# Kernel tuning notes

Hardware: AMD Instinct MI355X
Metric: run time of the kernel (lower is better)

## Reference

```python
import jax, jax.numpy as jnp
import numpy as np

NUM_HEADS = 16


def setup_inputs() -> dict:
    key = jax.random.key(0)
    ks = jax.random.split(key, 5)
    B, N, D = 2, 2048, 1024
    scale = 1.0 / np.sqrt(D)  # roughly xavier-ish magnitude for weights
    return {
        "x": jax.random.normal(ks[0], (B, N, D), dtype=jnp.float32),
        "W_query": jax.random.normal(ks[1], (D, D), dtype=jnp.float32) * scale,
        "W_key": jax.random.normal(ks[2], (D, D), dtype=jnp.float32) * scale,
        "W_value": jax.random.normal(ks[3], (D, D), dtype=jnp.float32) * scale,
        "W_output": jax.random.normal(ks[4], (D, D), dtype=jnp.float32) * scale,
    }


def reference(x, W_query, W_key, W_value, W_output):
    # x: [B, N, D]; weights: [D, D]
    B, N, D = x.shape
    H = NUM_HEADS
    hd = D // H

    def mh_embed(W):
        # linear_embedding then split heads: [B, N, D] -> [B, H, N, hd]
        y = jnp.einsum("bnd,de->bne", x, W)
        return y.reshape(B, N, H, hd).transpose(0, 2, 1, 3)

    q = mh_embed(W_query)
    k = mh_embed(W_key)
    v = mh_embed(W_value)

    # NOTE: source scales by token_dim**-0.5 (full model dim), not head_dim
    attn = jnp.einsum("bhnd,bhmd->bhnm", q, k) * (D ** -0.5)
    attn = jax.nn.softmax(attn, axis=-1)
    out = jnp.einsum("bhnm,bhmd->bhnd", attn, v)  # [B, H, N, hd]

    out = out.transpose(0, 2, 1, 3).reshape(B, N, D)  # merge heads
    out = jnp.einsum("bnd,de->bne", out, W_output)
    return out
```

## Files before the change

### kernel.cpp

```cpp
#include <hip/hip_runtime.h>

#define D_MODEL 1024
#define N_TOK   2048
#define NHEAD   16
#define HDIM    64
#define BATCH   2
#define M_TOT   (BATCH*N_TOK)

typedef unsigned short u16;
typedef __bf16 bf16x8 __attribute__((ext_vector_type(8)));
typedef float  f32x4  __attribute__((ext_vector_type(4)));

#define QSCALE 0.04508422002777439f

__device__ __forceinline__ u16 f2bf(float f) {
  union { float f; unsigned u; } v; v.f = f;
  unsigned r = v.u + 0x7fffu + ((v.u >> 16) & 1u);
  return (u16)(r >> 16);
}

__device__ __forceinline__ float bf2f(u16 u) {
  union { unsigned u; float f; } v; v.u = ((unsigned)u) << 16; return v.f;
}

__device__ __forceinline__ unsigned pk2bf(float a, float b) {
#if __has_builtin(__builtin_amdgcn_cvt_pk_bf16_f32)
  typedef __bf16 bf16x2_t __attribute__((ext_vector_type(2)));
  bf16x2_t r = __builtin_amdgcn_cvt_pk_bf16_f32(a, b);
  union { bf16x2_t v; unsigned u; } c; c.v = r; return c.u;
#else
  return (unsigned)f2bf(a) | ((unsigned)f2bf(b) << 16);
#endif
}

__device__ __forceinline__ void gl2lds16(const void* g, void* l) {
  __builtin_amdgcn_global_load_lds(
      (__attribute__((address_space(1))) void*)g,
      (__attribute__((address_space(3))) void*)l, 16, 0, 0);
}

__global__ void prep_kernel(const float* __restrict__ x,
                            const float* __restrict__ s0, const float* __restrict__ s1,
                            const float* __restrict__ s2, const float* __restrict__ s3,
                            u16* __restrict__ xb,
                            u16* __restrict__ d0, u16* __restrict__ d1,
                            u16* __restrict__ d2, u16* __restrict__ d3) {
  const int t = threadIdx.y * 32 + threadIdx.x;
  if (blockIdx.z == 4) {
    int base = (blockIdx.y * 32 + blockIdx.x) * 256 + t;
#pragma unroll
    for (int r = 0; r < 4; ++r) {
      int i = base + r * 262144;
      float4 v = ((const float4*)x)[i];
      ushort4 o;
      o.x = f2bf(v.x); o.y = f2bf(v.y); o.z = f2bf(v.z); o.w = f2bf(v.w);
      ((ushort4*)xb)[i] = o;
    }
    return;
  }
  const float* src; u16* dst;
  switch (blockIdx.z) {
    case 0:  src = s0; dst = d0; break;
    case 1:  src = s1; dst = d1; break;
    case 2:  src = s2; dst = d2; break;
    default: src = s3; dst = d3; break;
  }
  float sc = (blockIdx.z == 0) ? QSCALE : 1.0f;
  __shared__ float tile[32][33];
  int xg = blockIdx.x * 32 + threadIdx.x;
  int ybase = blockIdx.y * 32;
#pragma unroll
  for (int r = 0; r < 4; ++r)
    tile[threadIdx.y + r*8][threadIdx.x] = src[(size_t)(ybase + threadIdx.y + r*8)*D_MODEL + xg];
  __syncthreads();
#pragma unroll
  for (int r = 0; r < 4; ++r)
    dst[(size_t)(blockIdx.x*32 + threadIdx.y + r*8)*D_MODEL + ybase + threadIdx.x] =
        f2bf(tile[threadIdx.x][threadIdx.y + r*8] * sc);
}

__device__ __forceinline__ void gemm_body(const u16* __restrict__ A,
                                          const u16* __restrict__ Bt,
                                          void* __restrict__ Cout, int mode) {
  __shared__ __attribute__((aligned(16))) u16 lA[2][128*32];
  __shared__ __attribute__((aligned(16))) u16 lB[2][128*32];
  const int t = threadIdx.x;
  const int lane = t & 63, w = t >> 6;
  const int wm = w >> 1, wn = w & 1;
  const int q4 = lane >> 4, l15 = lane & 15;
  const int m0 = blockIdx.y * 128, n0 = blockIdx.x * 128;

  const int c0 = t, c1 = 256 + t;
  const int r0 = c0 >> 2, g0 = (c0 & 3) ^ (r0 & 3);
  const int r1 = c1 >> 2, g1 = (c1 & 3) ^ (r1 & 3);

  f32x4 acc[4][4] = {};

  gl2lds16(A  + (size_t)(m0 + r0)*D_MODEL + g0*8, &lA[0][c0*8]);
  gl2lds16(Bt + (size_t)(n0 + r0)*D_MODEL + g0*8, &lB[0][c0*8]);
  gl2lds16(A  + (size_t)(m0 + r1)*D_MODEL + g1*8, &lA[0][c1*8]);
  gl2lds16(Bt + (size_t)(n0 + r1)*D_MODEL + g1*8, &lB[0][c1*8]);

  for (int it = 0; it < 32; ++it) {
    const int cur = it & 1;
    __syncthreads();
    if (it + 1 < 32) {
      const int kn = (it + 1) * 32;
      u16* dA = &lA[cur ^ 1][0]; u16* dB = &lB[cur ^ 1][0];
      gl2lds16(A  + (size_t)(m0 + r0)*D_MODEL + kn + g0*8, dA + c0*8);
      gl2lds16(Bt + (size_t)(n0 + r0)*D_MODEL + kn + g0*8, dB + c0*8);
      gl2lds16(A  + (size_t)(m0 + r1)*D_MODEL + kn + g1*8, dA + c1*8);
      gl2lds16(Bt + (size_t)(n0 + r1)*D_MODEL + kn + g1*8, dB + c1*8);
    }
    const u16* sA = &lA[cur][0]; const u16* sB = &lB[cur][0];
    bf16x8 af[4], bfr[4];
#pragma unroll
    for (int mi = 0; mi < 4; ++mi) {
      int r = wm*64 + mi*16 + l15;
      af[mi] = *(const bf16x8*)(sA + r*32 + ((q4 ^ (r & 3)) * 8));
    }
#pragma unroll
    for (int ni = 0; ni < 4; ++ni) {
      int r = wn*64 + ni*16 + l15;
      bfr[ni] = *(const bf16x8*)(sB + r*32 + ((q4 ^ (r & 3)) * 8));
    }
#pragma unroll
    for (int mi = 0; mi < 4; ++mi)
#pragma unroll
      for (int ni = 0; ni < 4; ++ni)
        acc[mi][ni] = __builtin_amdgcn_mfma_f32_16x16x32_bf16(af[mi], bfr[ni], acc[mi][ni], 0, 0, 0);
  }

#pragma unroll
  for (int mi = 0; mi < 4; ++mi) {
#pragma unroll
    for (int ni = 0; ni < 4; ++ni) {
      const int tok0 = m0 + wm*64 + mi*16 + q4*4;
      const int col  = n0 + wn*64 + ni*16 + l15;
      if (mode == 0) {
        u16* D = (u16*)Cout;
#pragma unroll
        for (int r = 0; r < 4; ++r) {
          int tok = tok0 + r;
          int b = tok >> 11, n = tok & (N_TOK-1);
          int h = col >> 6, d = col & (HDIM-1);
          D[(((size_t)(b*NHEAD + h))*N_TOK + n)*HDIM + d] = f2bf(acc[mi][ni][r]);
        }
      } else {
        int b = tok0 >> 11, n = tok0 & (N_TOK-1);
        int h = col >> 6, d = col & (HDIM-1);
        ushort4 pk;
        pk.x = f2bf(acc[mi][ni][0]); pk.y = f2bf(acc[mi][ni][1]);
        pk.z = f2bf(acc[mi][ni][2]); pk.w = f2bf(acc[mi][ni][3]);
        *(ushort4*)((u16*)Cout + ((size_t)(b*NHEAD + h)*HDIM + d)*N_TOK + n) = pk;
      }
    }
  }
}

__global__ __launch_bounds__(256) void qkv_kernel(const u16* __restrict__ xb,
    const u16* __restrict__ wqt, const u16* __restrict__ wkt, const u16* __restrict__ wvt,
    u16* __restrict__ Q, u16* __restrict__ K, u16* __restrict__ Vt) {
  int z = blockIdx.z;
  const u16* B = (z == 0) ? wqt : (z == 1) ? wkt : wvt;
  void* C = (z == 0) ? (void*)Q : (z == 1) ? (void*)K : (void*)Vt;
  gemm_body(xb, B, C, (z == 2) ? 2 : 0);
}

__global__ __launch_bounds__(256) void out_kernel(const u16* __restrict__ ctx,
    const u16* __restrict__ wot, float* __restrict__ out) {
  __shared__ __attribute__((aligned(16))) u16 lA[2][64*32];
  __shared__ __attribute__((aligned(16))) u16 lB[2][128*32];
  const int t = threadIdx.x;
  const int lane = t & 63, w = t >> 6;
  const int wm = w >> 1, wn = w & 1;
  const int q4 = lane >> 4, l15 = lane & 15;
  const int m0 = blockIdx.y * 64, n0 = blockIdx.x * 128;

  const int rA = t >> 2, gA = (t & 3) ^ (rA & 3);
  const int c0 = t, c1 = 256 + t;
  const int r0 = c0 >> 2, g0 = (c0 & 3) ^ (r0 & 3);
  const int r1 = c1 >> 2, g1 = (c1 & 3) ^ (r1 & 3);

  f32x4 acc[2][4] = {};

  gl2lds16(ctx + (size_t)(m0 + rA)*D_MODEL + gA*8, &lA[0][t*8]);
  gl2lds16(wot + (size_t)(n0 + r0)*D_MODEL + g0*8, &lB[0][c0*8]);
  gl2lds16(wot + (size_t)(n0 + r1)*D_MODEL + g1*8, &lB[0][c1*8]);

  for (int it = 0; it < 32; ++it) {
    const int cur = it & 1;
    __syncthreads();
    if (it + 1 < 32) {
      const int kn = (it + 1) * 32;
      u16* dA = &lA[cur ^ 1][0]; u16* dB = &lB[cur ^ 1][0];
      gl2lds16(ctx + (size_t)(m0 + rA)*D_MODEL + kn + gA*8, dA + t*8);
      gl2lds16(wot + (size_t)(n0 + r0)*D_MODEL + kn + g0*8, dB + c0*8);
      gl2lds16(wot + (size_t)(n0 + r1)*D_MODEL + kn + g1*8, dB + c1*8);
    }
    const u16* sA = &lA[cur][0]; const u16* sB = &lB[cur][0];
    bf16x8 af[2], bfr[4];
#pragma unroll
    for (int mi = 0; mi < 2; ++mi) {
      int r = wm*32 + mi*16 + l15;
      af[mi] = *(const bf16x8*)(sA + r*32 + ((q4 ^ (r & 3)) * 8));
    }
#pragma unroll
    for (int ni = 0; ni < 4; ++ni) {
      int r = wn*64 + ni*16 + l15;
      bfr[ni] = *(const bf16x8*)(sB + r*32 + ((q4 ^ (r & 3)) * 8));
    }
#pragma unroll
    for (int mi = 0; mi < 2; ++mi)
#pragma unroll
      for (int ni = 0; ni < 4; ++ni)
        acc[mi][ni] = __builtin_amdgcn_mfma_f32_16x16x32_bf16(af[mi], bfr[ni], acc[mi][ni], 0, 0, 0);
  }

#pragma unroll
  for (int mi = 0; mi < 2; ++mi) {
#pragma unroll
    for (int ni = 0; ni < 4; ++ni) {
      const int tok0 = m0 + wm*32 + mi*16 + q4*4;
      const int col  = n0 + wn*64 + ni*16 + l15;
#pragma unroll
      for (int r = 0; r < 4; ++r)
        out[(size_t)(tok0 + r)*D_MODEL + col] = acc[mi][ni][r];
    }
  }
}

__global__ __launch_bounds__(256, 4) void attn_kernel(const u16* __restrict__ Qg,
    const u16* __restrict__ Kg, const u16* __restrict__ Vtg,
    u16* __restrict__ Opart, float* __restrict__ Lpart) {
  __shared__ __attribute__((aligned(16))) u16 lds[16384];
  const int t = threadIdx.x;
  const int lane = t & 63, w = t >> 6;
  const int q4 = lane >> 4, l15 = lane & 15;
  const int q4sw = ((q4 & 1) << 1) | (q4 >> 1);
  const int bh = blockIdx.y;
  const int qb = blockIdx.x >> 1, half = blockIdx.x & 1;
  const int qw0 = qb * 128 + w * 32;
  const size_t kvBase = (size_t)bh * (N_TOK * HDIM);

  const int ck0 = t, ck1 = 256 + t;
  const int kr0 = ck0 >> 3, kg0 = (ck0 & 7) ^ (kr0 & 7);
  const int kr1 = ck1 >> 3, kg1 = (ck1 & 7) ^ (kr1 & 7);

  bf16x8 qf[2][2];
#pragma unroll
  for (int ni = 0; ni < 2; ++ni)
#pragma unroll
    for (int kk = 0; kk < 2; ++kk)
      qf[ni][kk] = *(const bf16x8*)(Qg + kvBase +
                    (size_t)(qw0 + ni*16 + l15)*HDIM + kk*32 + q4*8);

  f32x4 accO[4][2] = {};
  f32x4 accL[2] = {};
  const f32x4 fzero = {0.f, 0.f, 0.f, 0.f};
  union { unsigned uu[4]; bf16x8 v; } onesU;
  onesU.uu[0] = 0x3F803F80u; onesU.uu[1] = 0x3F803F80u;
  onesU.uu[2] = 0x3F803F80u; onesU.uu[3] = 0x3F803F80u;
  const bf16x8 ones = onesU.v;

  const int kvStart = half * 1024;
  gl2lds16(Kg  + kvBase + (size_t)(kvStart + kr0)*HDIM + kg0*8, lds + ck0*8);
  gl2lds16(Kg  + kvBase + (size_t)(kvStart + kr1)*HDIM + kg1*8, lds + ck1*8);
  gl2lds16(Vtg + kvBase + (size_t)kr0*N_TOK + kvStart + kg0*8,  lds + 8192 + ck0*8);
  gl2lds16(Vtg + kvBase + (size_t)kr1*N_TOK + kvStart + kg1*8,  lds + 8192 + ck1*8);

  for (int it = 0; it < 16; ++it) {
    const int cur = it & 1;
    __syncthreads();
    if (it + 1 < 16) {
      const int kvn = kvStart + (it + 1) * 64;
      u16* dK = lds + (cur ^ 1) * 4096;
      u16* dV = lds + 8192 + (cur ^ 1) * 4096;
      gl2lds16(Kg  + kvBase + (size_t)(kvn + kr0)*HDIM + kg0*8, dK + ck0*8);
      gl2lds16(Kg  + kvBase + (size_t)(kvn + kr1)*HDIM + kg1*8, dK + ck1*8);
      gl2lds16(Vtg + kvBase + (size_t)kr0*N_TOK + kvn + kg0*8,  dV + ck0*8);
      gl2lds16(Vtg + kvBase + (size_t)kr1*N_TOK + kvn + kg1*8,  dV + ck1*8);
    }
    const u16* sK = lds + cur * 4096;
    const u16* sV = lds + 8192 + cur * 4096;

    unsigned wv[4][2][2];
#pragma unroll
    for (int mip = 0; mip < 4; ++mip) {
      const int kv = mip*16 + l15;
      __builtin_amdgcn_s_setprio(1);
      bf16x8 a0 = *(const bf16x8*)(sK + kv*64 + (((q4    ) ^ (l15 & 7)) * 8));
      bf16x8 a1 = *(const bf16x8*)(sK + kv*64 + (((4 + q4) ^ (l15 & 7)) * 8));
      f32x4 s0, s1;
      s0 = __builtin_amdgcn_mfma_f32_16x16x32_bf16(a0, qf[0][0], fzero, 0, 0, 0);
      s1 = __builtin_amdgcn_mfma_f32_16x16x32_bf16(a0, qf[1][0], fzero, 0, 0, 0);
      s0 = __builtin_amdgcn_mfma_f32_16x16x32_bf16(a1, qf[0][1], s0, 0, 0, 0);
      s1 = __builtin_amdgcn_mfma_f32_16x16x32_bf16(a1, qf[1][1], s1, 0, 0, 0);
      __builtin_amdgcn_s_setprio(0);
      wv[mip][0][0] = pk2bf(__builtin_amdgcn_exp2f(s0[0]), __builtin_amdgcn_exp2f(s0[1]));
      wv[mip][0][1] = pk2bf(__builtin_amdgcn_exp2f(s0[2]), __builtin_amdgcn_exp2f(s0[3]));
      wv[mip][1][0] = pk2bf(__builtin_amdgcn_exp2f(s1[0]), __builtin_amdgcn_exp2f(s1[1]));
      wv[mip][1][1] = pk2bf(__builtin_amdgcn_exp2f(s1[2]), __builtin_amdgcn_exp2f(s1[3]));
    }

    bf16x8 bp[2][2];
#pragma unroll
    for (int ni = 0; ni < 2; ++ni)
#pragma unroll
      for (int kk2 = 0; kk2 < 2; ++kk2) {
        unsigned x0 = wv[2*kk2][ni][0], x1 = wv[2*kk2][ni][1];
        unsigned y0 = wv[2*kk2+1][ni][0], y1 = wv[2*kk2+1][ni][1];
        asm("v_permlane16_swap_b32 %0, %1" : "+v"(x0), "+v"(y0));
        asm("v_permlane16_swap_b32 %0, %1" : "+v"(x1), "+v"(y1));
        union { unsigned u[4]; bf16x8 v; } pb;
        pb.u[0] = x0; pb.u[1] = x1; pb.u[2] = y0; pb.u[3] = y1;
        bp[ni][kk2] = pb.v;
      }

    __builtin_amdgcn_s_setprio(1);
#pragma unroll
    for (int kk2 = 0; kk2 < 2; ++kk2) {
      accL[0] = __builtin_amdgcn_mfma_f32_16x16x32_bf16(ones, bp[0][kk2], accL[0], 0, 0, 0);
      accL[1] = __builtin_amdgcn_mfma_f32_16x16x32_bf16(ones, bp[1][kk2], accL[1], 0, 0, 0);
#pragma unroll
      for (int mi2 = 0; mi2 < 4; ++mi2) {
        const int d = mi2*16 + l15;
        bf16x8 av = *(const bf16x8*)(sV + d*64 + (((kk2*4 + q4sw) ^ (d & 7)) * 8));
#pragma unroll
        for (int ni = 0; ni < 2; ++ni)
          accO[mi2][ni] = __builtin_amdgcn_mfma_f32_16x16x32_bf16(av, bp[ni][kk2], accO[mi2][ni], 0, 0, 0);
      }
    }
    __builtin_amdgcn_s_setprio(0);
  }

  const int b = bh >> 4, head = bh & (NHEAD-1);
  u16* Obase = Opart + (size_t)half * (M_TOT * D_MODEL);
#pragma unroll
  for (int ni = 0; ni < 2; ++ni) {
    const int q = qw0 + ni*16 + l15;
    if (q4 == 0)
      Lpart[(size_t)half*(32*N_TOK) + bh*N_TOK + q] = accL[ni][0];
    const size_t rb = ((size_t)(b*N_TOK + q))*D_MODEL + head*HDIM + q4*4;
#pragma unroll
    for (int mi2 = 0; mi2 < 4; ++mi2) {
      uint2 u;
      u.x = pk2bf(accO[mi2][ni][0], accO[mi2][ni][1]);
      u.y = pk2bf(accO[mi2][ni][2], accO[mi2][ni][3]);
      *(uint2*)(Obase + rb + mi2*16) = u;
    }
  }
}

__global__ __launch_bounds__(256) void combine_kernel(const u16* __restrict__ Opart,
    const float* __restrict__ Lpart, u16* __restrict__ ctx) {
  int i = blockIdx.x * 256 + threadIdx.x;
  int tok = i >> 7, c8 = i & 127;
  int n = tok & (N_TOK-1), b = tok >> 11;
  int h = c8 >> 3;
  int bh = b*NHEAD + h;
  float l = Lpart[(size_t)bh*N_TOK + n] + Lpart[(size_t)(32*N_TOK) + bh*N_TOK + n];
  float inv = 1.0f / l;
  const size_t off = (size_t)tok*D_MODEL + c8*8;
  ushort4 a0 = *(const ushort4*)(Opart + off);
  ushort4 a1 = *(const ushort4*)(Opart + off + 4);
  ushort4 b0 = *(const ushort4*)(Opart + (size_t)(M_TOT*D_MODEL) + off);
  ushort4 b1 = *(const ushort4*)(Opart + (size_t)(M_TOT*D_MODEL) + off + 4);
  uint2 o0, o1;
  o0.x = pk2bf((bf2f(a0.x)+bf2f(b0.x))*inv, (bf2f(a0.y)+bf2f(b0.y))*inv);
  o0.y = pk2bf((bf2f(a0.z)+bf2f(b0.z))*inv, (bf2f(a0.w)+bf2f(b0.w))*inv);
  o1.x = pk2bf((bf2f(a1.x)+bf2f(b1.x))*inv, (bf2f(a1.y)+bf2f(b1.y))*inv);
  o1.y = pk2bf((bf2f(a1.z)+bf2f(b1.z))*inv, (bf2f(a1.w)+bf2f(b1.w))*inv);
  *(uint2*)(ctx + off) = o0;
  *(uint2*)(ctx + off + 4) = o1;
}

extern "C" void kernel_launch(void* const* d_in, const int* in_sizes, int n_in,
                              void* d_out, int out_size, void* d_ws, size_t ws_size,
                              hipStream_t stream) {
  const float* x  = (const float*)d_in[0];
  const float* Wq = (const float*)d_in[1];
  const float* Wk = (const float*)d_in[2];
  const float* Wv = (const float*)d_in[3];
  const float* Wo = (const float*)d_in[4];
  float* out = (float*)d_out;

  char* ws = (char*)d_ws;
  u16* xb   = (u16*)(ws);
  u16* wqt  = (u16*)(ws + (8u  << 20));
  u16* wkt  = (u16*)(ws + (10u << 20));
  u16* wvt  = (u16*)(ws + (12u << 20));
  u16* wot  = (u16*)(ws + (14u << 20));
  u16* Qw   = (u16*)(ws + (16u << 20));
  u16* Kw   = (u16*)(ws + (24u << 20));
  u16* Vtw  = (u16*)(ws + (32u << 20));
  u16* ctx  = (u16*)(ws + (40u << 20));
  u16* Op   = (u16*)(ws + (48u << 20));
  float* Lp = (float*)(ws + (64u << 20));
  (void)in_sizes; (void)n_in; (void)out_size; (void)ws_size;

  prep_kernel<<<dim3(32, 32, 5), dim3(32, 8), 0, stream>>>(x, Wq, Wk, Wv, Wo,
                                                           xb, wqt, wkt, wvt, wot);
  qkv_kernel<<<dim3(8, 32, 3), 256, 0, stream>>>(xb, wqt, wkt, wvt, Qw, Kw, Vtw);
  attn_kernel<<<dim3(32, 32), 256, 0, stream>>>(Qw, Kw, Vtw, Op, Lp);
  combine_kernel<<<2048, 256, 0, stream>>>(Op, Lp, ctx);
  out_kernel<<<dim3(8, 64), 256, 0, stream>>>(ctx, wot, out);
}
```

Baseline: 202.0 us.

## Load K and V fragments directly from global memory instead of LDS staging

```diff
diff --git a/kernel.cpp b/kernel.cpp
--- a/kernel.cpp
+++ b/kernel.cpp
@@ -233,7 +233,6 @@
 __global__ __launch_bounds__(256, 4) void attn_kernel(const u16* __restrict__ Qg,
     const u16* __restrict__ Kg, const u16* __restrict__ Vtg,
     u16* __restrict__ Opart, float* __restrict__ Lpart) {
-  __shared__ __attribute__((aligned(16))) u16 lds[16384];
   const int t = threadIdx.x;
   const int lane = t & 63, w = t >> 6;
   const int q4 = lane >> 4, l15 = lane & 15;
@@ -242,10 +241,8 @@
   const int qb = blockIdx.x >> 1, half = blockIdx.x & 1;
   const int qw0 = qb * 128 + w * 32;
   const size_t kvBase = (size_t)bh * (N_TOK * HDIM);
-
-  const int ck0 = t, ck1 = 256 + t;
-  const int kr0 = ck0 >> 3, kg0 = (ck0 & 7) ^ (kr0 & 7);
-  const int kr1 = ck1 >> 3, kg1 = (ck1 & 7) ^ (kr1 & 7);
+  const u16* __restrict__ Kbh = Kg + kvBase;
+  const u16* __restrict__ Vbh = Vtg + kvBase;
 
   bf16x8 qf[2][2];
 #pragma unroll
@@ -264,33 +261,17 @@
   const bf16x8 ones = onesU.v;
 
   const int kvStart = half * 1024;
-  gl2lds16(Kg  + kvBase + (size_t)(kvStart + kr0)*HDIM + kg0*8, lds + ck0*8);
-  gl2lds16(Kg  + kvBase + (size_t)(kvStart + kr1)*HDIM + kg1*8, lds + ck1*8);
-  gl2lds16(Vtg + kvBase + (size_t)kr0*N_TOK + kvStart + kg0*8,  lds + 8192 + ck0*8);
-  gl2lds16(Vtg + kvBase + (size_t)kr1*N_TOK + kvStart + kg1*8,  lds + 8192 + ck1*8);
 
   for (int it = 0; it < 16; ++it) {
-    const int cur = it & 1;
-    __syncthreads();
-    if (it + 1 < 16) {
-      const int kvn = kvStart + (it + 1) * 64;
-      u16* dK = lds + (cur ^ 1) * 4096;
-      u16* dV = lds + 8192 + (cur ^ 1) * 4096;
-      gl2lds16(Kg  + kvBase + (size_t)(kvn + kr0)*HDIM + kg0*8, dK + ck0*8);
-      gl2lds16(Kg  + kvBase + (size_t)(kvn + kr1)*HDIM + kg1*8, dK + ck1*8);
-      gl2lds16(Vtg + kvBase + (size_t)kr0*N_TOK + kvn + kg0*8,  dV + ck0*8);
-      gl2lds16(Vtg + kvBase + (size_t)kr1*N_TOK + kvn + kg1*8,  dV + ck1*8);
-    }
-    const u16* sK = lds + cur * 4096;
-    const u16* sV = lds + 8192 + cur * 4096;
+    const int kv0 = kvStart + it * 64;
 
     unsigned wv[4][2][2];
 #pragma unroll
     for (int mip = 0; mip < 4; ++mip) {
-      const int kv = mip*16 + l15;
+      const u16* krow = Kbh + (size_t)(kv0 + mip*16 + l15) * HDIM;
+      bf16x8 a0 = *(const bf16x8*)(krow + q4*8);
+      bf16x8 a1 = *(const bf16x8*)(krow + 32 + q4*8);
       __builtin_amdgcn_s_setprio(1);
-      bf16x8 a0 = *(const bf16x8*)(sK + kv*64 + (((q4    ) ^ (l15 & 7)) * 8));
-      bf16x8 a1 = *(const bf16x8*)(sK + kv*64 + (((4 + q4) ^ (l15 & 7)) * 8));
       f32x4 s0, s1;
       s0 = __builtin_amdgcn_mfma_f32_16x16x32_bf16(a0, qf[0][0], fzero, 0, 0, 0);
       s1 = __builtin_amdgcn_mfma_f32_16x16x32_bf16(a0, qf[1][0], fzero, 0, 0, 0);
@@ -317,21 +298,21 @@
         bp[ni][kk2] = pb.v;
       }
 
-    __builtin_amdgcn_s_setprio(1);
 #pragma unroll
     for (int kk2 = 0; kk2 < 2; ++kk2) {
+      const u16* vcol = Vbh + kv0 + kk2*32 + q4sw*8;
+      __builtin_amdgcn_s_setprio(1);
       accL[0] = __builtin_amdgcn_mfma_f32_16x16x32_bf16(ones, bp[0][kk2], accL[0], 0, 0, 0);
       accL[1] = __builtin_amdgcn_mfma_f32_16x16x32_bf16(ones, bp[1][kk2], accL[1], 0, 0, 0);
 #pragma unroll
       for (int mi2 = 0; mi2 < 4; ++mi2) {
-        const int d = mi2*16 + l15;
-        bf16x8 av = *(const bf16x8*)(sV + d*64 + (((kk2*4 + q4sw) ^ (d & 7)) * 8));
+        bf16x8 av = *(const bf16x8*)(vcol + (size_t)(mi2*16 + l15) * N_TOK);
 #pragma unroll
         for (int ni = 0; ni < 2; ++ni)
           accO[mi2][ni] = __builtin_amdgcn_mfma_f32_16x16x32_bf16(av, bp[ni][kk2], accO[mi2][ni], 0, 0, 0);
       }
-    }
-    __builtin_amdgcn_s_setprio(0);
+      __builtin_amdgcn_s_setprio(0);
+    }
   }
 
   const int b = bh >> 4, head = bh & (NHEAD-1);
```

Measured after the change: 271.3 us. 1.34x slower.

## Fuse split-attention combine into output projection A-tile loading

Applied to the files above, without the earlier changes.

```diff
diff --git a/kernel.cpp b/kernel.cpp
--- a/kernel.cpp
+++ b/kernel.cpp
@@ -31,6 +31,13 @@
 #else
   return (unsigned)f2bf(a) | ((unsigned)f2bf(b) << 16);
 #endif
+}
+
+__device__ __forceinline__ unsigned comb2(unsigned a, unsigned b, float inv) {
+  union { unsigned u; float f; } al, ah, bl, bh2;
+  al.u = a << 16; ah.u = a & 0xffff0000u;
+  bl.u = b << 16; bh2.u = b & 0xffff0000u;
+  return pk2bf((al.f + bl.f) * inv, (ah.f + bh2.f) * inv);
 }
 
 __device__ __forceinline__ void gl2lds16(const void* g, void* l) {
@@ -167,8 +174,9 @@
   gemm_body(xb, B, C, (z == 2) ? 2 : 0);
 }
 
-__global__ __launch_bounds__(256) void out_kernel(const u16* __restrict__ ctx,
-    const u16* __restrict__ wot, float* __restrict__ out) {
+__global__ __launch_bounds__(256) void out_kernel(const u16* __restrict__ Opart,
+    const float* __restrict__ Lpart, const u16* __restrict__ wot,
+    float* __restrict__ out) {
   __shared__ __attribute__((aligned(16))) u16 lA[2][64*32];
   __shared__ __attribute__((aligned(16))) u16 lB[2][128*32];
   const int t = threadIdx.x;
@@ -178,23 +186,43 @@
   const int m0 = blockIdx.y * 64, n0 = blockIdx.x * 128;
 
   const int rA = t >> 2, gA = (t & 3) ^ (rA & 3);
+  const int tokA = m0 + rA;
+  const int bA = tokA >> 11, nA = tokA & (N_TOK-1);
+  const int lbase = bA*NHEAD*N_TOK + nA;
+  const size_t oBase = (size_t)tokA*D_MODEL + gA*8;
+
   const int c0 = t, c1 = 256 + t;
   const int r0 = c0 >> 2, g0 = (c0 & 3) ^ (r0 & 3);
   const int r1 = c1 >> 2, g1 = (c1 & 3) ^ (r1 & 3);
 
   f32x4 acc[2][4] = {};
 
-  gl2lds16(ctx + (size_t)(m0 + rA)*D_MODEL + gA*8, &lA[0][t*8]);
+  {
+    uint4 o0 = *(const uint4*)(Opart + oBase);
+    uint4 o1 = *(const uint4*)(Opart + (size_t)(M_TOT*D_MODEL) + oBase);
+    float l0 = Lpart[lbase];
+    float l1 = Lpart[32*N_TOK + lbase];
+    float inv = 1.0f / (l0 + l1);
+    uint4 res;
+    res.x = comb2(o0.x, o1.x, inv); res.y = comb2(o0.y, o1.y, inv);
+    res.z = comb2(o0.z, o1.z, inv); res.w = comb2(o0.w, o1.w, inv);
+    *(uint4*)(&lA[0][t*8]) = res;
+  }
   gl2lds16(wot + (size_t)(n0 + r0)*D_MODEL + g0*8, &lB[0][c0*8]);
   gl2lds16(wot + (size_t)(n0 + r1)*D_MODEL + g1*8, &lB[0][c1*8]);
 
   for (int it = 0; it < 32; ++it) {
     const int cur = it & 1;
     __syncthreads();
+    uint4 o0, o1; float l0 = 0.f, l1 = 0.f;
     if (it + 1 < 32) {
       const int kn = (it + 1) * 32;
-      u16* dA = &lA[cur ^ 1][0]; u16* dB = &lB[cur ^ 1][0];
-      gl2lds16(ctx + (size_t)(m0 + rA)*D_MODEL + kn + gA*8, dA + t*8);
+      o0 = *(const uint4*)(Opart + oBase + kn);
+      o1 = *(const uint4*)(Opart + (size_t)(M_TOT*D_MODEL) + oBase + kn);
+      const int head = (it + 1) >> 1;
+      l0 = Lpart[head*N_TOK + lbase];
+      l1 = Lpart[32*N_TOK + head*N_TOK + lbase];
+      u16* dB = &lB[cur ^ 1][0];
       gl2lds16(wot + (size_t)(n0 + r0)*D_MODEL + kn + g0*8, dB + c0*8);
       gl2lds16(wot + (size_t)(n0 + r1)*D_MODEL + kn + g1*8, dB + c1*8);
     }
@@ -215,6 +243,13 @@
 #pragma unroll
       for (int ni = 0; ni < 4; ++ni)
         acc[mi][ni] = __builtin_amdgcn_mfma_f32_16x16x32_bf16(af[mi], bfr[ni], acc[mi][ni], 0, 0, 0);
+    if (it + 1 < 32) {
+      float inv = 1.0f / (l0 + l1);
+      uint4 res;
+      res.x = comb2(o0.x, o1.x, inv); res.y = comb2(o0.y, o1.y, inv);
+      res.z = comb2(o0.z, o1.z, inv); res.w = comb2(o0.w, o1.w, inv);
+      *(uint4*)(&lA[cur ^ 1][t*8]) = res;
+    }
   }
 
 #pragma unroll
@@ -352,29 +387,6 @@
   }
 }
 
-__global__ __launch_bounds__(256) void combine_kernel(const u16* __restrict__ Opart,
-    const float* __restrict__ Lpart, u16* __restrict__ ctx) {
-  int i = blockIdx.x * 256 + threadIdx.x;
-  int tok = i >> 7, c8 = i & 127;
-  int n = tok & (N_TOK-1), b = tok >> 11;
-  int h = c8 >> 3;
-  int bh = b*NHEAD + h;
-  float l = Lpart[(size_t)bh*N_TOK + n] + Lpart[(size_t)(32*N_TOK) + bh*N_TOK + n];
-  float inv = 1.0f / l;
-  const size_t off = (size_t)tok*D_MODEL + c8*8;
-  ushort4 a0 = *(const ushort4*)(Opart + off);
-  ushort4 a1 = *(const ushort4*)(Opart + off + 4);
-  ushort4 b0 = *(const ushort4*)(Opart + (size_t)(M_TOT*D_MODEL) + off);
-  ushort4 b1 = *(const ushort4*)(Opart + (size_t)(M_TOT*D_MODEL) + off + 4);
-  uint2 o0, o1;
-  o0.x = pk2bf((bf2f(a0.x)+bf2f(b0.x))*inv, (bf2f(a0.y)+bf2f(b0.y))*inv);
-  o0.y = pk2bf((bf2f(a0.z)+bf2f(b0.z))*inv, (bf2f(a0.w)+bf2f(b0.w))*inv);
-  o1.x = pk2bf((bf2f(a1.x)+bf2f(b1.x))*inv, (bf2f(a1.y)+bf2f(b1.y))*inv);
-  o1.y = pk2bf((bf2f(a1.z)+bf2f(b1.z))*inv, (bf2f(a1.w)+bf2f(b1.w))*inv);
-  *(uint2*)(ctx + off) = o0;
-  *(uint2*)(ctx + off + 4) = o1;
-}
-
 extern "C" void kernel_launch(void* const* d_in, const int* in_sizes, int n_in,
                               void* d_out, int out_size, void* d_ws, size_t ws_size,
                               hipStream_t stream) {
@@ -394,7 +406,6 @@
   u16* Qw   = (u16*)(ws + (16u << 20));
   u16* Kw   = (u16*)(ws + (24u << 20));
   u16* Vtw  = (u16*)(ws + (32u << 20));
-  u16* ctx  = (u16*)(ws + (40u << 20));
   u16* Op   = (u16*)(ws + (48u << 20));
   float* Lp = (float*)(ws + (64u << 20));
   (void)in_sizes; (void)n_in; (void)out_size; (void)ws_size;
@@ -403,6 +414,5 @@
                                                            xb, wqt, wkt, wvt, wot);
   qkv_kernel<<<dim3(8, 32, 3), 256, 0, stream>>>(xb, wqt, wkt, wvt, Qw, Kw, Vtw);
   attn_kernel<<<dim3(32, 32), 256, 0, stream>>>(Qw, Kw, Vtw, Op, Lp);
-  combine_kernel<<<2048, 256, 0, stream>>>(Op, Lp, ctx);
-  out_kernel<<<dim3(8, 64), 256, 0, stream>>>(ctx, wot, out);
-}
+  out_kernel<<<dim3(8, 64), 256, 0, stream>>>(Op, Lp, wot, out);
+}
```

After: 202.1 us. No clear change (+0.1%).
